# Kernel tuning notes

Measured on AMD Instinct MI355X. Metric: run time of the kernel, lower is better.

The kernel has to match this reference:

```python
import jax, jax.numpy as jnp
import numpy as np

N = 100000        # nodes
E = 3200000       # edges (avg degree 32)
IN_F = 128
OUT_F = 64
ALPHA = 0.2       # LeakyReLU negative slope
EPS = 1e-5        # LayerNorm eps


def setup_inputs() -> dict:
    key = jax.random.key(0)
    k = jax.random.split(key, 5)
    x = jax.random.normal(k[0], (N, IN_F), jnp.float32)
    edge = jax.random.randint(k[1], (2, E), 0, N, dtype=jnp.int32)
    # kaiming-normal inits as in the torch module
    W = jax.random.normal(k[2], (OUT_F, IN_F), jnp.float32) * np.float32(np.sqrt(2.0 / IN_F))
    b = jnp.zeros((OUT_F,), jnp.float32)
    a = jax.random.normal(k[3], (2 * OUT_F,), jnp.float32) * np.float32(np.sqrt(2.0 / (2 * OUT_F)))
    gamma = jnp.ones((OUT_F,), jnp.float32)
    beta = jnp.zeros((OUT_F,), jnp.float32)
    return {"x": x, "edge": edge, "W": W, "b": b, "a": a, "gamma": gamma, "beta": beta}


def reference(x, edge, W, b, a, gamma, beta):
    # h = Linear(in->out)
    h = x @ W.T + b                                   # [N, OUT_F]
    src, dst = edge[0], edge[1]
    # edge score a · cat(h[src], h[dst]) == (h @ a_l)[src] + (h @ a_r)[dst]
    sl = h @ a[:OUT_F]                                # [N]
    sr = h @ a[OUT_F:]                                # [N]
    score = sl[src] + sr[dst]                         # [E]
    lrelu = jnp.where(score > 0, score, ALPHA * score)
    edge_e = jnp.exp(-lrelu)                          # [E] (dropout=0 / eval)
    # sparse spmm: h_prime[i] = sum_{e: src_e==i} edge_e * h[dst_e]
    msg = edge_e[:, None] * h[dst]                    # [E, OUT_F]
    h_prime = jax.ops.segment_sum(msg, src, num_segments=N)  # [N, OUT_F]
    # LayerNorm over feature dim (biased variance, as torch)
    mu = jnp.mean(h_prime, axis=-1, keepdims=True)
    var = jnp.mean(jnp.square(h_prime - mu), axis=-1, keepdims=True)
    h_norm = (h_prime - mu) * jax.lax.rsqrt(var + EPS) * gamma + beta
    # concat=True -> ELU
    return jax.nn.elu(h_norm)
```

## Files before the change

kernel.cpp:

```cpp
#include <hip/hip_runtime.h>
#include <hip/hip_fp16.h>
#include <cstdint>
#include <cstddef>

#define INF_  128
#define OUTF  64
#define ALPHA 0.2f
#define LN_EPS 1e-5f

#define NBLK  512
#define LOCB  6
#define LOCN  64
#define CAP   3072
#define NBKMAX 1600

typedef __attribute__((ext_vector_type(8))) _Float16 half8;
typedef __attribute__((ext_vector_type(4))) float    f32x4;

__global__ __launch_bounds__(256) void gemm_kernel(
    const float* __restrict__ x, const float* __restrict__ W,
    const float* __restrict__ b, const float* __restrict__ a,
    __half* __restrict__ hh, float* __restrict__ sl, float* __restrict__ sr, int n)
{
    __shared__ half8 wfrag_lds[16][64];

    const int tid  = threadIdx.x;
    const int lane = tid & 63;
    const int wv   = tid >> 6;
    const int col  = lane & 15;
    const int quad = lane >> 4;

    for (int idx = tid; idx < 1024; idx += 256) {
        const int l  = idx & 63, ct = idx >> 6;
        const int c  = ct >> 2,  t  = ct & 3;
        const int row = 4 * (l & 15) + t;
        const int k0  = 32 * c + 8 * (l >> 4);
        const float4 f0 = ((const float4*)W)[row * 32 + (k0 >> 2)];
        const float4 f1 = ((const float4*)W)[row * 32 + (k0 >> 2) + 1];
        half8 h;
        h[0] = (_Float16)f0.x; h[1] = (_Float16)f0.y;
        h[2] = (_Float16)f0.z; h[3] = (_Float16)f0.w;
        h[4] = (_Float16)f1.x; h[5] = (_Float16)f1.y;
        h[6] = (_Float16)f1.z; h[7] = (_Float16)f1.w;
        wfrag_lds[ct][l] = h;
    }
    __syncthreads();

    half8 bf[4][4];
    #pragma unroll
    for (int c = 0; c < 4; c++)
        #pragma unroll
        for (int t = 0; t < 4; t++)
            bf[c][t] = wfrag_lds[c * 4 + t][lane];

    const float4 b4  = ((const float4*)b)[col];
    const float4 al4 = ((const float4*)a)[col];
    const float4 ar4 = ((const float4*)a)[16 + col];

    const int ntile  = (n + 15) >> 4;
    const int wgid   = blockIdx.x * 4 + wv;
    const int nwaves = gridDim.x * 4;

    for (int tile = wgid; tile < ntile; tile += nwaves) {
        const int node0 = tile << 4;
        const int xr    = min(node0 + col, n - 1);
        const float* xrow = x + (size_t)xr * INF_ + 8 * quad;

        f32x4 acc0 = {0,0,0,0}, acc1 = {0,0,0,0}, acc2 = {0,0,0,0}, acc3 = {0,0,0,0};
        #pragma unroll
        for (int c = 0; c < 4; c++) {
            const float4 f0 = *(const float4*)(xrow + 32 * c);
            const float4 f1 = *(const float4*)(xrow + 32 * c + 4);
            half8 af;
            af[0] = (_Float16)f0.x; af[1] = (_Float16)f0.y;
            af[2] = (_Float16)f0.z; af[3] = (_Float16)f0.w;
            af[4] = (_Float16)f1.x; af[5] = (_Float16)f1.y;
            af[6] = (_Float16)f1.z; af[7] = (_Float16)f1.w;
            acc0 = __builtin_amdgcn_mfma_f32_16x16x32_f16(af, bf[c][0], acc0, 0, 0, 0);
            acc1 = __builtin_amdgcn_mfma_f32_16x16x32_f16(af, bf[c][1], acc1, 0, 0, 0);
            acc2 = __builtin_amdgcn_mfma_f32_16x16x32_f16(af, bf[c][2], acc2, 0, 0, 0);
            acc3 = __builtin_amdgcn_mfma_f32_16x16x32_f16(af, bf[c][3], acc3, 0, 0, 0);
        }

        #pragma unroll
        for (int reg = 0; reg < 4; reg++) {
            const int node = node0 + quad * 4 + reg;
            const float v0 = acc0[reg] + b4.x;
            const float v1 = acc1[reg] + b4.y;
            const float v2 = acc2[reg] + b4.z;
            const float v3 = acc3[reg] + b4.w;
            float p = v0 * al4.x + v1 * al4.y + v2 * al4.z + v3 * al4.w;
            float q = v0 * ar4.x + v1 * ar4.y + v2 * ar4.z + v3 * ar4.w;
            p += __shfl_xor(p, 1); p += __shfl_xor(p, 2);
            p += __shfl_xor(p, 4); p += __shfl_xor(p, 8);
            q += __shfl_xor(q, 1); q += __shfl_xor(q, 2);
            q += __shfl_xor(q, 4); q += __shfl_xor(q, 8);
            if (node < n) {
                ushort4 u;
                u.x = __half_as_ushort(__float2half(v0));
                u.y = __half_as_ushort(__float2half(v1));
                u.z = __half_as_ushort(__float2half(v2));
                u.w = __half_as_ushort(__float2half(v3));
                ((ushort4*)hh)[(size_t)node * 16 + col] = u;
                if (col == 0) { sl[node] = p; sr[node] = q; }
            }
        }
    }
}

__global__ __launch_bounds__(256) void scatter_reserve(
    const int* __restrict__ src, const int* __restrict__ dst,
    int* __restrict__ gcnt, int* __restrict__ pk, int E, int nbk)
{
    __shared__ int hist[NBKMAX];
    const int t = threadIdx.x;
    for (int i = t; i < nbk; i += 256) hist[i] = 0;
    __syncthreads();

    const int chunk = (((E + NBLK - 1) / NBLK) + 7) & ~7;
    const int lo = blockIdx.x * chunk;
    const int hi = min(E, lo + chunk);

    for (int e = lo + t * 8; e < hi; e += 2048) {
        if (e + 7 < hi) {
            const int4 a4 = *(const int4*)(src + e);
            const int4 c4 = *(const int4*)(src + e + 4);
            atomicAdd(&hist[a4.x >> LOCB], 1);
            atomicAdd(&hist[a4.y >> LOCB], 1);
            atomicAdd(&hist[a4.z >> LOCB], 1);
            atomicAdd(&hist[a4.w >> LOCB], 1);
            atomicAdd(&hist[c4.x >> LOCB], 1);
            atomicAdd(&hist[c4.y >> LOCB], 1);
            atomicAdd(&hist[c4.z >> LOCB], 1);
            atomicAdd(&hist[c4.w >> LOCB], 1);
        } else {
            for (int k = e; k < hi; k++) atomicAdd(&hist[src[k] >> LOCB], 1);
        }
    }
    __syncthreads();

    for (int i = t; i < nbk; i += 256) {
        const int c = hist[i];
        hist[i] = c ? atomicAdd(&gcnt[i], c) : 0;
    }
    __syncthreads();

    for (int e = lo + t * 8; e < hi; e += 2048) {
        if (e + 7 < hi) {
            const int4 s4 = *(const int4*)(src + e);
            const int4 t4 = *(const int4*)(src + e + 4);
            const int4 d4 = *(const int4*)(dst + e);
            const int4 u4 = *(const int4*)(dst + e + 4);
            int p;
            p = atomicAdd(&hist[s4.x >> LOCB], 1); if (p < CAP) pk[(size_t)(s4.x >> LOCB) * CAP + p] = ((s4.x & 63) << 17) | d4.x;
            p = atomicAdd(&hist[s4.y >> LOCB], 1); if (p < CAP) pk[(size_t)(s4.y >> LOCB) * CAP + p] = ((s4.y & 63) << 17) | d4.y;
            p = atomicAdd(&hist[s4.z >> LOCB], 1); if (p < CAP) pk[(size_t)(s4.z >> LOCB) * CAP + p] = ((s4.z & 63) << 17) | d4.z;
            p = atomicAdd(&hist[s4.w >> LOCB], 1); if (p < CAP) pk[(size_t)(s4.w >> LOCB) * CAP + p] = ((s4.w & 63) << 17) | d4.w;
            p = atomicAdd(&hist[t4.x >> LOCB], 1); if (p < CAP) pk[(size_t)(t4.x >> LOCB) * CAP + p] = ((t4.x & 63) << 17) | u4.x;
            p = atomicAdd(&hist[t4.y >> LOCB], 1); if (p < CAP) pk[(size_t)(t4.y >> LOCB) * CAP + p] = ((t4.y & 63) << 17) | u4.y;
            p = atomicAdd(&hist[t4.z >> LOCB], 1); if (p < CAP) pk[(size_t)(t4.z >> LOCB) * CAP + p] = ((t4.z & 63) << 17) | u4.z;
            p = atomicAdd(&hist[t4.w >> LOCB], 1); if (p < CAP) pk[(size_t)(t4.w >> LOCB) * CAP + p] = ((t4.w & 63) << 17) | u4.w;
        } else {
            for (int k = e; k < hi; k++) {
                const int s = src[k];
                const int p = atomicAdd(&hist[s >> LOCB], 1);
                if (p < CAP) pk[(size_t)(s >> LOCB) * CAP + p] = ((s & 63) << 17) | dst[k];
            }
        }
    }
}

__global__ __launch_bounds__(256) void gat_fused(
    const int* __restrict__ pk, const int* __restrict__ gcnt,
    const float* __restrict__ sl, const float* __restrict__ sr,
    const __half* __restrict__ hh,
    const float* __restrict__ gamma, const float* __restrict__ beta,
    float* __restrict__ out, int n)
{
    __shared__ int    ldst[CAP];
    __shared__ __half lwgt[CAP];
    __shared__ float  lsl[LOCN];
    __shared__ int    lhist[LOCN];
    __shared__ int    lbase[LOCN + 1];
    __shared__ int    cur2[LOCN];

    const int B     = blockIdx.x;
    const int t     = threadIdx.x;
    const int lane  = t & 63;
    const int wv    = t >> 6;
    const int fgrp  = lane & 15;
    const int equad = lane >> 4;

    if (t < LOCN) {
        lhist[t] = 0;
        const int s = (B << LOCB) + t;
        lsl[t] = (s < n) ? sl[s] : 0.f;
    }
    const int cnt = min(gcnt[B], CAP);
    const size_t base0 = (size_t)B * CAP;
    __syncthreads();

    for (int j = t; j < cnt; j += 256)
        atomicAdd(&lhist[(pk[base0 + j] >> 17) & (LOCN - 1)], 1);
    __syncthreads();

    if (wv == 0) {
        const int v = lhist[lane];
        int s = v;
        #pragma unroll
        for (int d = 1; d < 64; d <<= 1) {
            const int u = __shfl(s, lane - d);
            if (lane >= d) s += u;
        }
        lbase[lane] = s - v;
        cur2[lane]  = s - v;
        if (lane == 63) lbase[64] = s;
    }
    __syncthreads();

    for (int j = t; j < cnt; j += 256) {
        const int v = pk[base0 + j];
        const int s = (v >> 17) & (LOCN - 1);
        const int d = v & 0x1FFFF;
        const float sc = lsl[s] + sr[d];
        const float lr = sc > 0.f ? sc : ALPHA * sc;
        const int p = atomicAdd(&cur2[s], 1);
        ldst[p] = d;
        lwgt[p] = __float2half(__expf(-lr));
    }
    __syncthreads();

    const float4 gm4 = ((const float4*)gamma)[fgrp];
    const float4 bt4 = ((const float4*)beta)[fgrp];

    for (int k = wv; k < LOCN; k += 4) {
        const int node = (B << LOCB) + k;
        const int nb   = lbase[k];
        const int len  = lbase[k + 1] - nb;

        float4 acc = make_float4(0.f, 0.f, 0.f, 0.f);

        int e0 = equad, e1 = 4 + equad;
        int dA = 0, dB = 0; float wA = 0.f, wB = 0.f;
        if (e0 < len) { dA = ldst[nb + e0]; wA = __half2float(lwgt[nb + e0]); }
        if (e1 < len) { dB = ldst[nb + e1]; wB = __half2float(lwgt[nb + e1]); }
        uint2 uA = ((const uint2*)hh)[(size_t)dA * 16 + fgrp];
        uint2 uB = ((const uint2*)hh)[(size_t)dB * 16 + fgrp];

        for (int tt = 0; tt < len; tt += 8) {
            uint2 nA = make_uint2(0u, 0u), nB = make_uint2(0u, 0u);
            float nwA = 0.f, nwB = 0.f;
            if (tt + 8 < len) {
                const int f0 = tt + 8 + equad, f1 = tt + 12 + equad;
                int xA = 0, xB = 0;
                if (f0 < len) { xA = ldst[nb + f0]; nwA = __half2float(lwgt[nb + f0]); }
                if (f1 < len) { xB = ldst[nb + f1]; nwB = __half2float(lwgt[nb + f1]); }
                nA = ((const uint2*)hh)[(size_t)xA * 16 + fgrp];
                nB = ((const uint2*)hh)[(size_t)xB * 16 + fgrp];
            }
            const float2 fA0 = __half22float2(*(const __half2*)&uA.x);
            const float2 fA1 = __half22float2(*(const __half2*)&uA.y);
            const float2 fB0 = __half22float2(*(const __half2*)&uB.x);
            const float2 fB1 = __half22float2(*(const __half2*)&uB.y);
            acc.x = fmaf(wA, fA0.x, acc.x); acc.y = fmaf(wA, fA0.y, acc.y);
            acc.z = fmaf(wA, fA1.x, acc.z); acc.w = fmaf(wA, fA1.y, acc.w);
            acc.x = fmaf(wB, fB0.x, acc.x); acc.y = fmaf(wB, fB0.y, acc.y);
            acc.z = fmaf(wB, fB1.x, acc.z); acc.w = fmaf(wB, fB1.y, acc.w);
            uA = nA; uB = nB; wA = nwA; wB = nwB;
        }

        acc.x += __shfl_xor(acc.x, 16); acc.x += __shfl_xor(acc.x, 32);
        acc.y += __shfl_xor(acc.y, 16); acc.y += __shfl_xor(acc.y, 32);
        acc.z += __shfl_xor(acc.z, 16); acc.z += __shfl_xor(acc.z, 32);
        acc.w += __shfl_xor(acc.w, 16); acc.w += __shfl_xor(acc.w, 32);

        float s1 = acc.x + acc.y + acc.z + acc.w;
        float s2 = acc.x * acc.x + acc.y * acc.y + acc.z * acc.z + acc.w * acc.w;
        #pragma unroll
        for (int dd = 1; dd < 16; dd <<= 1) {
            s1 += __shfl_xor(s1, dd);
            s2 += __shfl_xor(s2, dd);
        }
        const float mu  = s1 * (1.f / 64.f);
        const float var = fmaxf(s2 * (1.f / 64.f) - mu * mu, 0.f);
        const float rs  = rsqrtf(var + LN_EPS);

        float4 y;
        y.x = (acc.x - mu) * rs * gm4.x + bt4.x;
        y.y = (acc.y - mu) * rs * gm4.y + bt4.y;
        y.z = (acc.z - mu) * rs * gm4.z + bt4.z;
        y.w = (acc.w - mu) * rs * gm4.w + bt4.w;
        y.x = y.x > 0.f ? y.x : __expf(y.x) - 1.f;
        y.y = y.y > 0.f ? y.y : __expf(y.y) - 1.f;
        y.z = y.z > 0.f ? y.z : __expf(y.z) - 1.f;
        y.w = y.w > 0.f ? y.w : __expf(y.w) - 1.f;
        if (node < n && equad == 0)
            ((float4*)out)[(size_t)node * 16 + fgrp] = y;
    }
}

extern "C" void kernel_launch(void* const* d_in, const int* in_sizes, int n_in,
                              void* d_out, int out_size, void* d_ws, size_t ws_size,
                              hipStream_t stream)
{
    const float* x     = (const float*)d_in[0];
    const int*   edge  = (const int*)  d_in[1];
    const float* W     = (const float*)d_in[2];
    const float* b     = (const float*)d_in[3];
    const float* a     = (const float*)d_in[4];
    const float* gamma = (const float*)d_in[5];
    const float* beta  = (const float*)d_in[6];
    float* out = (float*)d_out;

    const int n = in_sizes[0] / INF_;
    const int E = in_sizes[1] / 2;
    const int* src = edge;
    const int* dst = edge + E;
    const int nbk = (n + LOCN - 1) >> LOCB;

    char* ws = (char*)d_ws;
    size_t offb = 0;
    auto alloc = [&](size_t bytes) -> void* {
        void* p = ws + offb;
        offb = (offb + bytes + 255) & ~(size_t)255;
        return p;
    };
    __half* hh   = (__half*)alloc((size_t)n * OUTF * 2);
    float*  sl   = (float*) alloc((size_t)n * 4);
    float*  sr   = (float*) alloc((size_t)n * 4);
    int*    gcnt = (int*)   alloc((size_t)nbk * 4);
    int*    pk   = (int*)   alloc((size_t)nbk * CAP * 4);

    hipMemsetAsync(gcnt, 0, (size_t)nbk * 4, stream);
    hipLaunchKernelGGL(scatter_reserve, dim3(NBLK), dim3(256), 0, stream, src, dst, gcnt, pk, E, nbk);
    hipLaunchKernelGGL(gemm_kernel,     dim3(1024), dim3(256), 0, stream, x, W, b, a, hh, sl, sr, n);
    hipLaunchKernelGGL(gat_fused,       dim3(nbk),  dim3(256), 0, stream, pk, gcnt, sl, sr, hh, gamma, beta, out, n);
}
```

Before: 255.4 us.

## Replace one-pass bucket scatter with two-level partition scatter and register-cached edge pass

Edge bucketing is split into two stages. First, a coarse partition by src>>9 into per-block private segments, with no global atomics. Second, a pass that scatters each partition into the 64-node buckets using global atomics on gcnt. The fused GAT kernel moves to 512 threads and keeps each edge's packed value, rank and weight in registers, so pk is read once and the second atomic pass over a cursor array is gone. The aim is to cut global atomic contention and redundant reads of pk, in exchange for an extra kernel launch, an extra round-trip through the pka buffer, and fixed PCAP/MAXK caps that silently drop edges if a partition or bucket overflows.

Result: slower. 569.9 us (+123.2%).

```diff
diff --git a/kernel.cpp b/kernel.cpp
--- a/kernel.cpp
+++ b/kernel.cpp
@@ -8,11 +8,13 @@
 #define ALPHA 0.2f
 #define LN_EPS 1e-5f
 
-#define NBLK  512
+#define PBLK  256
+#define NPART 196
+#define PCAP  112
 #define LOCB  6
 #define LOCN  64
 #define CAP   3072
-#define NBKMAX 1600
+#define MAXK  6
 
 typedef __attribute__((ext_vector_type(8))) _Float16 half8;
 typedef __attribute__((ext_vector_type(4))) float    f32x4;
@@ -108,69 +110,70 @@
     }
 }
 
-__global__ __launch_bounds__(256) void scatter_reserve(
+__global__ __launch_bounds__(1024) void part_scatter(
     const int* __restrict__ src, const int* __restrict__ dst,
-    int* __restrict__ gcnt, int* __restrict__ pk, int E, int nbk)
-{
-    __shared__ int hist[NBKMAX];
+    int* __restrict__ pka, int* __restrict__ acnt, int E)
+{
+    __shared__ int lcur[NPART];
     const int t = threadIdx.x;
-    for (int i = t; i < nbk; i += 256) hist[i] = 0;
-    __syncthreads();
-
-    const int chunk = (((E + NBLK - 1) / NBLK) + 7) & ~7;
-    const int lo = blockIdx.x * chunk;
+    const int b = blockIdx.x;
+    if (t < NPART) lcur[t] = 0;
+    __syncthreads();
+
+    const int chunk = (E + PBLK - 1) / PBLK;
+    const int lo = b * chunk;
     const int hi = min(E, lo + chunk);
 
-    for (int e = lo + t * 8; e < hi; e += 2048) {
-        if (e + 7 < hi) {
-            const int4 a4 = *(const int4*)(src + e);
-            const int4 c4 = *(const int4*)(src + e + 4);
-            atomicAdd(&hist[a4.x >> LOCB], 1);
-            atomicAdd(&hist[a4.y >> LOCB], 1);
-            atomicAdd(&hist[a4.z >> LOCB], 1);
-            atomicAdd(&hist[a4.w >> LOCB], 1);
-            atomicAdd(&hist[c4.x >> LOCB], 1);
-            atomicAdd(&hist[c4.y >> LOCB], 1);
-            atomicAdd(&hist[c4.z >> LOCB], 1);
-            atomicAdd(&hist[c4.w >> LOCB], 1);
-        } else {
-            for (int k = e; k < hi; k++) atomicAdd(&hist[src[k] >> LOCB], 1);
-        }
-    }
-    __syncthreads();
-
-    for (int i = t; i < nbk; i += 256) {
-        const int c = hist[i];
-        hist[i] = c ? atomicAdd(&gcnt[i], c) : 0;
-    }
-    __syncthreads();
-
-    for (int e = lo + t * 8; e < hi; e += 2048) {
+    for (int e = lo + t * 8; e < hi; e += 8192) {
         if (e + 7 < hi) {
             const int4 s4 = *(const int4*)(src + e);
-            const int4 t4 = *(const int4*)(src + e + 4);
+            const int4 s5 = *(const int4*)(src + e + 4);
             const int4 d4 = *(const int4*)(dst + e);
-            const int4 u4 = *(const int4*)(dst + e + 4);
-            int p;
-            p = atomicAdd(&hist[s4.x >> LOCB], 1); if (p < CAP) pk[(size_t)(s4.x >> LOCB) * CAP + p] = ((s4.x & 63) << 17) | d4.x;
-            p = atomicAdd(&hist[s4.y >> LOCB], 1); if (p < CAP) pk[(size_t)(s4.y >> LOCB) * CAP + p] = ((s4.y & 63) << 17) | d4.y;
-            p = atomicAdd(&hist[s4.z >> LOCB], 1); if (p < CAP) pk[(size_t)(s4.z >> LOCB) * CAP + p] = ((s4.z & 63) << 17) | d4.z;
-            p = atomicAdd(&hist[s4.w >> LOCB], 1); if (p < CAP) pk[(size_t)(s4.w >> LOCB) * CAP + p] = ((s4.w & 63) << 17) | d4.w;
-            p = atomicAdd(&hist[t4.x >> LOCB], 1); if (p < CAP) pk[(size_t)(t4.x >> LOCB) * CAP + p] = ((t4.x & 63) << 17) | u4.x;
-            p = atomicAdd(&hist[t4.y >> LOCB], 1); if (p < CAP) pk[(size_t)(t4.y >> LOCB) * CAP + p] = ((t4.y & 63) << 17) | u4.y;
-            p = atomicAdd(&hist[t4.z >> LOCB], 1); if (p < CAP) pk[(size_t)(t4.z >> LOCB) * CAP + p] = ((t4.z & 63) << 17) | u4.z;
-            p = atomicAdd(&hist[t4.w >> LOCB], 1); if (p < CAP) pk[(size_t)(t4.w >> LOCB) * CAP + p] = ((t4.w & 63) << 17) | u4.w;
+            const int4 d5 = *(const int4*)(dst + e + 4);
+            int p, c;
+            p = s4.x >> 9; c = atomicAdd(&lcur[p], 1); if (c < PCAP) pka[(size_t)((p << 8) | b) * PCAP + c] = ((s4.x & 511) << 17) | d4.x;
+            p = s4.y >> 9; c = atomicAdd(&lcur[p], 1); if (c < PCAP) pka[(size_t)((p << 8) | b) * PCAP + c] = ((s4.y & 511) << 17) | d4.y;
+            p = s4.z >> 9; c = atomicAdd(&lcur[p], 1); if (c < PCAP) pka[(size_t)((p << 8) | b) * PCAP + c] = ((s4.z & 511) << 17) | d4.z;
+            p = s4.w >> 9; c = atomicAdd(&lcur[p], 1); if (c < PCAP) pka[(size_t)((p << 8) | b) * PCAP + c] = ((s4.w & 511) << 17) | d4.w;
+            p = s5.x >> 9; c = atomicAdd(&lcur[p], 1); if (c < PCAP) pka[(size_t)((p << 8) | b) * PCAP + c] = ((s5.x & 511) << 17) | d5.x;
+            p = s5.y >> 9; c = atomicAdd(&lcur[p], 1); if (c < PCAP) pka[(size_t)((p << 8) | b) * PCAP + c] = ((s5.y & 511) << 17) | d5.y;
+            p = s5.z >> 9; c = atomicAdd(&lcur[p], 1); if (c < PCAP) pka[(size_t)((p << 8) | b) * PCAP + c] = ((s5.z & 511) << 17) | d5.z;
+            p = s5.w >> 9; c = atomicAdd(&lcur[p], 1); if (c < PCAP) pka[(size_t)((p << 8) | b) * PCAP + c] = ((s5.w & 511) << 17) | d5.w;
         } else {
             for (int k = e; k < hi; k++) {
                 const int s = src[k];
-                const int p = atomicAdd(&hist[s >> LOCB], 1);
-                if (p < CAP) pk[(size_t)(s >> LOCB) * CAP + p] = ((s & 63) << 17) | dst[k];
+                const int p = s >> 9;
+                const int c = atomicAdd(&lcur[p], 1);
+                if (c < PCAP) pka[(size_t)((p << 8) | b) * PCAP + c] = ((s & 511) << 17) | dst[k];
             }
         }
     }
-}
-
-__global__ __launch_bounds__(256) void gat_fused(
+    __syncthreads();
+    if (t < NPART) acnt[t * PBLK + b] = min(lcur[t], PCAP);
+}
+
+__global__ __launch_bounds__(256) void bucket_scatter(
+    const int* __restrict__ pka, const int* __restrict__ acnt,
+    int* __restrict__ gcnt, int* __restrict__ pk)
+{
+    const int p  = blockIdx.x >> 3;
+    const int sg = (blockIdx.x & 7) * 32;
+    const int t  = threadIdx.x;
+    const int s  = sg + (t & 31);
+    const int q  = t >> 5;
+
+    const int len = acnt[p * PBLK + s];
+    const int* seg = pka + (size_t)(p * PBLK + s) * PCAP;
+    for (int i = q; i < len; i += 8) {
+        const int v  = seg[i];
+        const int s9 = v >> 17;
+        const int bk = (p << 3) | (s9 >> 6);
+        const int pos = atomicAdd(&gcnt[bk], 1);
+        if (pos < CAP) pk[(size_t)bk * CAP + pos] = ((s9 & 63) << 17) | (v & 0x1FFFF);
+    }
+}
+
+__global__ __launch_bounds__(512, 8) void gat_fused(
     const int* __restrict__ pk, const int* __restrict__ gcnt,
     const float* __restrict__ sl, const float* __restrict__ sr,
     const __half* __restrict__ hh,
@@ -182,7 +185,6 @@
     __shared__ float  lsl[LOCN];
     __shared__ int    lhist[LOCN];
     __shared__ int    lbase[LOCN + 1];
-    __shared__ int    cur2[LOCN];
 
     const int B     = blockIdx.x;
     const int t     = threadIdx.x;
@@ -200,8 +202,22 @@
     const size_t base0 = (size_t)B * CAP;
     __syncthreads();
 
-    for (int j = t; j < cnt; j += 256)
-        atomicAdd(&lhist[(pk[base0 + j] >> 17) & (LOCN - 1)], 1);
+    const int myn = (cnt > t) ? (cnt - t + 511) >> 9 : 0;
+    int   pkr[MAXK];
+    float wf[MAXK];
+    int   rk[MAXK];
+    #pragma unroll
+    for (int k = 0; k < MAXK; k++) {
+        if (k < myn) {
+            const int v = pk[base0 + t + (k << 9)];
+            pkr[k] = v;
+            const int s = (v >> 17) & (LOCN - 1);
+            rk[k] = atomicAdd(&lhist[s], 1);
+            const float sc = lsl[s] + sr[v & 0x1FFFF];
+            const float lr = sc > 0.f ? sc : ALPHA * sc;
+            wf[k] = __expf(-lr);
+        }
+    }
     __syncthreads();
 
     if (wv == 0) {
@@ -213,34 +229,33 @@
             if (lane >= d) s += u;
         }
         lbase[lane] = s - v;
-        cur2[lane]  = s - v;
         if (lane == 63) lbase[64] = s;
     }
     __syncthreads();
 
-    for (int j = t; j < cnt; j += 256) {
-        const int v = pk[base0 + j];
-        const int s = (v >> 17) & (LOCN - 1);
-        const int d = v & 0x1FFFF;
-        const float sc = lsl[s] + sr[d];
-        const float lr = sc > 0.f ? sc : ALPHA * sc;
-        const int p = atomicAdd(&cur2[s], 1);
-        ldst[p] = d;
-        lwgt[p] = __float2half(__expf(-lr));
+    #pragma unroll
+    for (int k = 0; k < MAXK; k++) {
+        if (k < myn) {
+            const int v = pkr[k];
+            const int s = (v >> 17) & (LOCN - 1);
+            const int p = lbase[s] + rk[k];
+            ldst[p] = v & 0x1FFFF;
+            lwgt[p] = __float2half(wf[k]);
+        }
     }
     __syncthreads();
 
     const float4 gm4 = ((const float4*)gamma)[fgrp];
     const float4 bt4 = ((const float4*)beta)[fgrp];
 
-    for (int k = wv; k < LOCN; k += 4) {
+    for (int k = wv; k < LOCN; k += 8) {
         const int node = (B << LOCB) + k;
         const int nb   = lbase[k];
         const int len  = lbase[k + 1] - nb;
 
         float4 acc = make_float4(0.f, 0.f, 0.f, 0.f);
 
-        int e0 = equad, e1 = 4 + equad;
+        const int e0 = equad, e1 = 4 + equad;
         int dA = 0, dB = 0; float wA = 0.f, wB = 0.f;
         if (e0 < len) { dA = ldst[nb + e0]; wA = __half2float(lwgt[nb + e0]); }
         if (e1 < len) { dB = ldst[nb + e1]; wB = __half2float(lwgt[nb + e1]); }
@@ -329,10 +344,13 @@
     float*  sl   = (float*) alloc((size_t)n * 4);
     float*  sr   = (float*) alloc((size_t)n * 4);
     int*    gcnt = (int*)   alloc((size_t)nbk * 4);
+    int*    acnt = (int*)   alloc((size_t)NPART * PBLK * 4);
+    int*    pka  = (int*)   alloc((size_t)NPART * PBLK * PCAP * 4);
     int*    pk   = (int*)   alloc((size_t)nbk * CAP * 4);
 
     hipMemsetAsync(gcnt, 0, (size_t)nbk * 4, stream);
-    hipLaunchKernelGGL(scatter_reserve, dim3(NBLK), dim3(256), 0, stream, src, dst, gcnt, pk, E, nbk);
-    hipLaunchKernelGGL(gemm_kernel,     dim3(1024), dim3(256), 0, stream, x, W, b, a, hh, sl, sr, n);
-    hipLaunchKernelGGL(gat_fused,       dim3(nbk),  dim3(256), 0, stream, pk, gcnt, sl, sr, hh, gamma, beta, out, n);
-}
+    hipLaunchKernelGGL(part_scatter,   dim3(PBLK),      dim3(1024), 0, stream, src, dst, pka, acnt, E);
+    hipLaunchKernelGGL(gemm_kernel,    dim3(1024),      dim3(256),  0, stream, x, W, b, a, hh, sl, sr, n);
+    hipLaunchKernelGGL(bucket_scatter, dim3(NPART * 8), dim3(256),  0, stream, pka, acnt, gcnt, pk);
+    hipLaunchKernelGGL(gat_fused,      dim3(nbk),       dim3(512),  0, stream, pk, gcnt, sl, sr, hh, gamma, beta, out, n);
+}
```

## Replace global-atomic bucket scatter with per-block LDS-sorted partition slabs

Applied to the files above, without the earlier changes.

The edge bucketing pass no longer reserves space with global atomics. Each of 256 blocks counting-sorts its edge chunk into 784 partitions of 128 source nodes in LDS and writes contiguous runs into fixed per-(partition, block) slabs of capacity 48. The fused aggregation kernel now handles 128 nodes per block with 512 threads, reading its slab with int4 loads and building the local CSR in LDS. This removes the memset and the global-atomic contention and gives more coalesced writes, in exchange for fixed-capacity slabs that silently drop edges on overflow and a larger workspace footprint.

Measured after the change: 250.9 us. About the same (-1.7%).

```diff
diff --git a/kernel.cpp b/kernel.cpp
--- a/kernel.cpp
+++ b/kernel.cpp
@@ -8,11 +8,14 @@
 #define ALPHA 0.2f
 #define LN_EPS 1e-5f
 
-#define NBLK  512
-#define LOCB  6
-#define LOCN  64
-#define CAP   3072
-#define NBKMAX 1600
+#define PBLK2 256
+#define BT2   512
+#define TILE  8192
+#define NP2   784
+#define NPS   1024
+#define PCAP2 48
+#define LOC2  128
+#define CSRCAP 4608
 
 typedef __attribute__((ext_vector_type(8))) _Float16 half8;
 typedef __attribute__((ext_vector_type(4))) float    f32x4;
@@ -108,81 +111,119 @@
     }
 }
 
-__global__ __launch_bounds__(256) void scatter_reserve(
+__global__ __launch_bounds__(512) void part_scatter(
     const int* __restrict__ src, const int* __restrict__ dst,
-    int* __restrict__ gcnt, int* __restrict__ pk, int E, int nbk)
+    int* __restrict__ pka, int* __restrict__ acnt, int E)
 {
-    __shared__ int hist[NBKMAX];
-    const int t = threadIdx.x;
-    for (int i = t; i < nbk; i += 256) hist[i] = 0;
-    __syncthreads();
-
-    const int chunk = (((E + NBLK - 1) / NBLK) + 7) & ~7;
-    const int lo = blockIdx.x * chunk;
+    __shared__ int hist[NPS];
+    __shared__ int bnd[NPS + 1];
+    __shared__ int cur[NPS];
+    __shared__ int gbase[NP2];
+    __shared__ int buf[TILE];
+    __shared__ int csum[16];
+    __shared__ int csb[16];
+
+    const int t    = threadIdx.x;
+    const int b    = blockIdx.x;
+    const int lane = t & 63;
+    const int wv   = t >> 6;
+
+    for (int i = t; i < NP2; i += 512) gbase[i] = 0;
+
+    const int chunk = (E + PBLK2 - 1) / PBLK2;
+    const int lo = b * chunk;
     const int hi = min(E, lo + chunk);
 
-    for (int e = lo + t * 8; e < hi; e += 2048) {
-        if (e + 7 < hi) {
-            const int4 a4 = *(const int4*)(src + e);
-            const int4 c4 = *(const int4*)(src + e + 4);
-            atomicAdd(&hist[a4.x >> LOCB], 1);
-            atomicAdd(&hist[a4.y >> LOCB], 1);
-            atomicAdd(&hist[a4.z >> LOCB], 1);
-            atomicAdd(&hist[a4.w >> LOCB], 1);
-            atomicAdd(&hist[c4.x >> LOCB], 1);
-            atomicAdd(&hist[c4.y >> LOCB], 1);
-            atomicAdd(&hist[c4.z >> LOCB], 1);
-            atomicAdd(&hist[c4.w >> LOCB], 1);
-        } else {
-            for (int k = e; k < hi; k++) atomicAdd(&hist[src[k] >> LOCB], 1);
-        }
-    }
-    __syncthreads();
-
-    for (int i = t; i < nbk; i += 256) {
-        const int c = hist[i];
-        hist[i] = c ? atomicAdd(&gcnt[i], c) : 0;
-    }
-    __syncthreads();
-
-    for (int e = lo + t * 8; e < hi; e += 2048) {
-        if (e + 7 < hi) {
-            const int4 s4 = *(const int4*)(src + e);
-            const int4 t4 = *(const int4*)(src + e + 4);
-            const int4 d4 = *(const int4*)(dst + e);
-            const int4 u4 = *(const int4*)(dst + e + 4);
-            int p;
-            p = atomicAdd(&hist[s4.x >> LOCB], 1); if (p < CAP) pk[(size_t)(s4.x >> LOCB) * CAP + p] = ((s4.x & 63) << 17) | d4.x;
-            p = atomicAdd(&hist[s4.y >> LOCB], 1); if (p < CAP) pk[(size_t)(s4.y >> LOCB) * CAP + p] = ((s4.y & 63) << 17) | d4.y;
-            p = atomicAdd(&hist[s4.z >> LOCB], 1); if (p < CAP) pk[(size_t)(s4.z >> LOCB) * CAP + p] = ((s4.z & 63) << 17) | d4.z;
-            p = atomicAdd(&hist[s4.w >> LOCB], 1); if (p < CAP) pk[(size_t)(s4.w >> LOCB) * CAP + p] = ((s4.w & 63) << 17) | d4.w;
-            p = atomicAdd(&hist[t4.x >> LOCB], 1); if (p < CAP) pk[(size_t)(t4.x >> LOCB) * CAP + p] = ((t4.x & 63) << 17) | u4.x;
-            p = atomicAdd(&hist[t4.y >> LOCB], 1); if (p < CAP) pk[(size_t)(t4.y >> LOCB) * CAP + p] = ((t4.y & 63) << 17) | u4.y;
-            p = atomicAdd(&hist[t4.z >> LOCB], 1); if (p < CAP) pk[(size_t)(t4.z >> LOCB) * CAP + p] = ((t4.z & 63) << 17) | u4.z;
-            p = atomicAdd(&hist[t4.w >> LOCB], 1); if (p < CAP) pk[(size_t)(t4.w >> LOCB) * CAP + p] = ((t4.w & 63) << 17) | u4.w;
-        } else {
-            for (int k = e; k < hi; k++) {
-                const int s = src[k];
-                const int p = atomicAdd(&hist[s >> LOCB], 1);
-                if (p < CAP) pk[(size_t)(s >> LOCB) * CAP + p] = ((s & 63) << 17) | dst[k];
+    for (int tb = lo; tb < hi; tb += TILE) {
+        const int tcnt = min(TILE, hi - tb);
+        for (int i = t; i < NPS; i += 512) hist[i] = 0;
+        __syncthreads();
+
+        int pp[16], pay[16];
+        #pragma unroll
+        for (int k = 0; k < 16; k++) {
+            const int e = tb + t + k * 512;
+            pp[k] = -1;
+            if (e < hi) {
+                const int s = src[e];
+                pp[k]  = s >> 7;
+                pay[k] = ((s & 127) << 17) | dst[e];
+                atomicAdd(&hist[pp[k]], 1);
             }
         }
-    }
+        __syncthreads();
+
+        int vA = hist[wv * 64 + lane];
+        int vB = hist[(wv + 8) * 64 + lane];
+        int sA = vA, sB = vB;
+        #pragma unroll
+        for (int d = 1; d < 64; d <<= 1) {
+            const int uA = __shfl(sA, lane - d);
+            const int uB = __shfl(sB, lane - d);
+            if (lane >= d) { sA += uA; sB += uB; }
+        }
+        if (lane == 63) { csum[wv] = sA; csum[wv + 8] = sB; }
+        __syncthreads();
+        if (t == 0) {
+            int r = 0;
+            #pragma unroll
+            for (int c2 = 0; c2 < 16; c2++) { csb[c2] = r; r += csum[c2]; }
+            bnd[NPS] = r;
+        }
+        __syncthreads();
+        {
+            const int eA = csb[wv] + sA - vA;
+            const int eB = csb[wv + 8] + sB - vB;
+            bnd[wv * 64 + lane]       = eA;
+            bnd[(wv + 8) * 64 + lane] = eB;
+            cur[wv * 64 + lane]       = eA;
+            cur[(wv + 8) * 64 + lane] = eB;
+        }
+        __syncthreads();
+
+        #pragma unroll
+        for (int k = 0; k < 16; k++) {
+            if (pp[k] >= 0) {
+                const int r = atomicAdd(&cur[pp[k]], 1);
+                buf[r] = pay[k];
+            }
+        }
+        __syncthreads();
+
+        for (int idx = t; idx < tcnt; idx += 512) {
+            int p = 0;
+            #pragma unroll
+            for (int step = 512; step >= 1; step >>= 1)
+                if (bnd[p + step] <= idx) p += step;
+            const int off = gbase[p] + (idx - bnd[p]);
+            if (off < PCAP2)
+                pka[(size_t)((p << 8) | b) * PCAP2 + off] = buf[idx];
+        }
+        __syncthreads();
+
+        for (int p = t; p < NP2; p += 512) gbase[p] += bnd[p + 1] - bnd[p];
+        __syncthreads();
+    }
+
+    for (int p = t; p < NP2; p += 512)
+        acnt[p * PBLK2 + b] = min(gbase[p], PCAP2);
 }
 
-__global__ __launch_bounds__(256) void gat_fused(
-    const int* __restrict__ pk, const int* __restrict__ gcnt,
+__global__ __launch_bounds__(512) void gat_fused(
+    const int* __restrict__ pka, const int* __restrict__ acnt,
     const float* __restrict__ sl, const float* __restrict__ sr,
     const __half* __restrict__ hh,
     const float* __restrict__ gamma, const float* __restrict__ beta,
     float* __restrict__ out, int n)
 {
-    __shared__ int    ldst[CAP];
-    __shared__ __half lwgt[CAP];
-    __shared__ float  lsl[LOCN];
-    __shared__ int    lhist[LOCN];
-    __shared__ int    lbase[LOCN + 1];
-    __shared__ int    cur2[LOCN];
+    __shared__ int    ldst[CSRCAP];
+    __shared__ __half lwgt[CSRCAP];
+    __shared__ int    alen[PBLK2];
+    __shared__ float  lsl[LOC2];
+    __shared__ int    lhist[LOC2];
+    __shared__ int    lbase[LOC2 + 1];
+    __shared__ int    cur2[LOC2];
+    __shared__ int    wtot_;
 
     const int B     = blockIdx.x;
     const int t     = threadIdx.x;
@@ -191,56 +232,88 @@
     const int fgrp  = lane & 15;
     const int equad = lane >> 4;
 
-    if (t < LOCN) {
+    for (int i = t; i < PBLK2; i += 512) alen[i] = acnt[B * PBLK2 + i];
+    if (t < LOC2) {
         lhist[t] = 0;
-        const int s = (B << LOCB) + t;
-        lsl[t] = (s < n) ? sl[s] : 0.f;
-    }
-    const int cnt = min(gcnt[B], CAP);
-    const size_t base0 = (size_t)B * CAP;
-    __syncthreads();
-
-    for (int j = t; j < cnt; j += 256)
-        atomicAdd(&lhist[(pk[base0 + j] >> 17) & (LOCN - 1)], 1);
-    __syncthreads();
-
-    if (wv == 0) {
-        const int v = lhist[lane];
-        int s = v;
+        const int g = (B << 7) + t;
+        lsl[t] = (g < n) ? sl[g] : 0.f;
+    }
+    __syncthreads();
+
+    const int4* slab4 = (const int4*)(pka + (size_t)(B << 8) * PCAP2);
+
+    for (int i = t; i < 3072; i += 512) {
+        const int j0  = i << 2;
+        const int seg = j0 / PCAP2;
+        const int off = j0 - seg * PCAP2;
+        const int m   = alen[seg] - off;
+        if (m > 0) {
+            const int4 v4 = slab4[i];
+            atomicAdd(&lhist[(v4.x >> 17) & 127], 1);
+            if (m > 1) atomicAdd(&lhist[(v4.y >> 17) & 127], 1);
+            if (m > 2) atomicAdd(&lhist[(v4.z >> 17) & 127], 1);
+            if (m > 3) atomicAdd(&lhist[(v4.w >> 17) & 127], 1);
+        }
+    }
+    __syncthreads();
+
+    int sv = 0, vv = 0;
+    if (t < 128) {
+        vv = lhist[t]; sv = vv;
         #pragma unroll
         for (int d = 1; d < 64; d <<= 1) {
-            const int u = __shfl(s, lane - d);
-            if (lane >= d) s += u;
-        }
-        lbase[lane] = s - v;
-        cur2[lane]  = s - v;
-        if (lane == 63) lbase[64] = s;
-    }
-    __syncthreads();
-
-    for (int j = t; j < cnt; j += 256) {
-        const int v = pk[base0 + j];
-        const int s = (v >> 17) & (LOCN - 1);
-        const int d = v & 0x1FFFF;
-        const float sc = lsl[s] + sr[d];
-        const float lr = sc > 0.f ? sc : ALPHA * sc;
-        const int p = atomicAdd(&cur2[s], 1);
-        ldst[p] = d;
-        lwgt[p] = __float2half(__expf(-lr));
+            const int u = __shfl(sv, lane - d);
+            if (lane >= d) sv += u;
+        }
+        if (t == 63) wtot_ = sv;
+    }
+    __syncthreads();
+    if (t < 128) {
+        const int base = (t >= 64) ? wtot_ : 0;
+        const int eb = base + sv - vv;
+        lbase[t] = eb; cur2[t] = eb;
+        if (t == 127) lbase[128] = base + sv;
+    }
+    __syncthreads();
+
+    for (int i = t; i < 3072; i += 512) {
+        const int j0  = i << 2;
+        const int seg = j0 / PCAP2;
+        const int off = j0 - seg * PCAP2;
+        const int m   = alen[seg] - off;
+        if (m > 0) {
+            const int4 v4 = slab4[i];
+            #pragma unroll
+            for (int c = 0; c < 4; c++) {
+                if (c < m) {
+                    const int v = (c == 0) ? v4.x : (c == 1) ? v4.y : (c == 2) ? v4.z : v4.w;
+                    const int s = (v >> 17) & 127;
+                    const int d = v & 0x1FFFF;
+                    const float sc = lsl[s] + sr[d];
+                    const float lr = sc > 0.f ? sc : ALPHA * sc;
+                    const int p = atomicAdd(&cur2[s], 1);
+                    if (p < CSRCAP) {
+                        ldst[p] = d;
+                        lwgt[p] = __float2half(__expf(-lr));
+                    }
+                }
+            }
+        }
     }
     __syncthreads();
 
     const float4 gm4 = ((const float4*)gamma)[fgrp];
     const float4 bt4 = ((const float4*)beta)[fgrp];
 
-    for (int k = wv; k < LOCN; k += 4) {
-        const int node = (B << LOCB) + k;
-        const int nb   = lbase[k];
-        const int len  = lbase[k + 1] - nb;
+    for (int k = wv; k < LOC2; k += 8) {
+        const int node = (B << 7) + k;
+        const int nb   = min(lbase[k], CSRCAP);
+        const int ne   = min(lbase[k + 1], CSRCAP);
+        const int len  = ne - nb;
 
         float4 acc = make_float4(0.f, 0.f, 0.f, 0.f);
 
-        int e0 = equad, e1 = 4 + equad;
+        const int e0 = equad, e1 = 4 + equad;
         int dA = 0, dB = 0; float wA = 0.f, wB = 0.f;
         if (e0 < len) { dA = ldst[nb + e0]; wA = __half2float(lwgt[nb + e0]); }
         if (e1 < len) { dB = ldst[nb + e1]; wB = __half2float(lwgt[nb + e1]); }
@@ -316,7 +389,7 @@
     const int E = in_sizes[1] / 2;
     const int* src = edge;
     const int* dst = edge + E;
-    const int nbk = (n + LOCN - 1) >> LOCB;
+    const int npart = (n + LOC2 - 1) >> 7;
 
     char* ws = (char*)d_ws;
     size_t offb = 0;
@@ -328,11 +401,10 @@
     __half* hh   = (__half*)alloc((size_t)n * OUTF * 2);
     float*  sl   = (float*) alloc((size_t)n * 4);
     float*  sr   = (float*) alloc((size_t)n * 4);
-    int*    gcnt = (int*)   alloc((size_t)nbk * 4);
-    int*    pk   = (int*)   alloc((size_t)nbk * CAP * 4);
-
-    hipMemsetAsync(gcnt, 0, (size_t)nbk * 4, stream);
-    hipLaunchKernelGGL(scatter_reserve, dim3(NBLK), dim3(256), 0, stream, src, dst, gcnt, pk, E, nbk);
-    hipLaunchKernelGGL(gemm_kernel,     dim3(1024), dim3(256), 0, stream, x, W, b, a, hh, sl, sr, n);
-    hipLaunchKernelGGL(gat_fused,       dim3(nbk),  dim3(256), 0, stream, pk, gcnt, sl, sr, hh, gamma, beta, out, n);
+    int*    acnt = (int*)   alloc((size_t)NP2 * PBLK2 * 4);
+    int*    pka  = (int*)   alloc((size_t)NP2 * PBLK2 * PCAP2 * 4);
+
+    hipLaunchKernelGGL(part_scatter, dim3(PBLK2), dim3(BT2), 0, stream, src, dst, pka, acnt, E);
+    hipLaunchKernelGGL(gemm_kernel,  dim3(1024),  dim3(256), 0, stream, x, W, b, a, hh, sl, sr, n);
+    hipLaunchKernelGGL(gat_fused,    dim3(npart), dim3(512), 0, stream, pka, acnt, sl, sr, hh, gamma, beta, out, n);
 }
```
